# Optimization experiments

Measured on AMD Instinct MI355X. Metric: run time of the kernel, lower is better.

## Reference

```python
import jax, jax.numpy as jnp
import numpy as np

B, CHAR_LEN, LSTM, VOCAB, NATTN = 4096, 64, 400, 73, 10

def _lstm_cell(x, h, c, W_ih, W_hh, b):
    # gates: [B, 4*LSTM] in (i, f, g, o) order, matching torch.nn.LSTMCell
    g = x @ W_ih.T + h @ W_hh.T + b
    i, f, gg, o = jnp.split(g, 4, axis=1)
    i = jax.nn.sigmoid(i); f = jax.nn.sigmoid(f)
    gg = jnp.tanh(gg); o = jax.nn.sigmoid(o)
    c_new = f * c + i * gg
    h_new = o * jnp.tanh(c_new)
    return h_new, c_new

def setup_inputs() -> dict:
    key = jax.random.key(0)
    ks = jax.random.split(key, 24)
    d = {}
    d['inputs'] = jax.random.normal(ks[0], (B, 3), jnp.float32)
    for n, k in zip(['h1','c1','h2','c2','h3','c3'], ks[1:7]):
        d[n] = jax.random.normal(k, (B, LSTM), jnp.float32) * 0.1
    d['kappa'] = jax.random.uniform(ks[7], (B, NATTN), jnp.float32) * 5.0
    d['w_prev'] = jax.random.uniform(ks[8], (B, VOCAB), jnp.float32)
    d['attention_values'] = jax.random.uniform(ks[9], (B, CHAR_LEN, VOCAB), jnp.float32)
    d['attention_lengths'] = jax.random.randint(ks[10], (B,), 1, CHAR_LEN + 1, jnp.int32)
    s = 0.05
    in1 = VOCAB + 3              # lstm1 input: [w, inputs]
    in23 = 3 + LSTM + VOCAB      # lstm2/3 input: [inputs, h, w]
    attn_in = VOCAB + 3 + LSTM
    d['W_ih1'] = jax.random.normal(ks[11], (4 * LSTM, in1), jnp.float32) * s
    d['W_hh1'] = jax.random.normal(ks[12], (4 * LSTM, LSTM), jnp.float32) * s
    d['b1'] = jax.random.normal(ks[13], (4 * LSTM,), jnp.float32) * s
    d['W_attn'] = jax.random.normal(ks[14], (3 * NATTN, attn_in), jnp.float32) * s
    d['b_attn'] = jax.random.normal(ks[15], (3 * NATTN,), jnp.float32) * s
    d['W_ih2'] = jax.random.normal(ks[16], (4 * LSTM, in23), jnp.float32) * s
    d['W_hh2'] = jax.random.normal(ks[17], (4 * LSTM, LSTM), jnp.float32) * s
    d['b2'] = jax.random.normal(ks[18], (4 * LSTM,), jnp.float32) * s
    d['W_ih3'] = jax.random.normal(ks[19], (4 * LSTM, in23), jnp.float32) * s
    d['W_hh3'] = jax.random.normal(ks[20], (4 * LSTM, LSTM), jnp.float32) * s
    d['b3'] = jax.random.normal(ks[21], (4 * LSTM,), jnp.float32) * s
    return d

def reference(inputs, h1, c1, h2, c2, h3, c3, kappa, w_prev, attention_values,
              attention_lengths, W_ih1, W_hh1, b1, W_attn, b_attn,
              W_ih2, W_hh2, b2, W_ih3, W_hh3, b3):
    char_len = attention_values.shape[1]
    # --- LSTM 1 ---
    s1_in = jnp.concatenate([w_prev, inputs], axis=1)
    h1n, c1n = _lstm_cell(s1_in, h1, c1, W_ih1, W_hh1, b1)
    # --- Gaussian-mixture location attention ---
    attn_in = jnp.concatenate([w_prev, inputs, h1n], axis=1)
    attn_params = jax.nn.softplus(attn_in @ W_attn.T + b_attn)
    alpha, beta, kap = jnp.split(attn_params, 3, axis=1)
    kap = kappa + kap / 25.0
    beta = jnp.maximum(beta, 0.01)
    u = jnp.arange(char_len, dtype=jnp.float32)[None, None, :]           # [1,1,C]
    phi = jnp.sum(alpha[:, :, None] *
                  jnp.exp(-jnp.square(kap[:, :, None] - u) / beta[:, :, None]),
                  axis=1)                                                 # [B,C]
    seq_mask = (jnp.arange(char_len)[None, :] < attention_lengths[:, None]).astype(jnp.float32)
    w = jnp.einsum('bc,bcv->bv', phi * seq_mask, attention_values)        # [B,V]
    # --- LSTM 2 & 3 ---
    s2_in = jnp.concatenate([inputs, h1n, w], axis=1)
    h2n, c2n = _lstm_cell(s2_in, h2, c2, W_ih2, W_hh2, b2)
    s3_in = jnp.concatenate([inputs, h2n, w], axis=1)
    h3n, c3n = _lstm_cell(s3_in, h3, c3, W_ih3, W_hh3, b3)
    return h3n
```

## Files before the change

### kernel.cpp

```cpp
#include <hip/hip_runtime.h>
#include <hip/hip_bf16.h>


#define B_SZ     4096
#define LSTM_N   400
#define NG       1600
#define VOCAB    73
#define NATTN    10
#define CHARLEN  64
#define KP1      512
#define KP23     896

typedef _Float16 half8 __attribute__((ext_vector_type(8)));
typedef __attribute__((ext_vector_type(4))) float floatx4;

__device__ __forceinline__ void gload_lds16(const void* g, void* l) {
    __builtin_amdgcn_global_load_lds(
        (const __attribute__((address_space(1))) void*)g,
        (__attribute__((address_space(3))) void*)l, 16, 0, 0);
}

__device__ __forceinline__ int lds_off(int r, int g) {
    return (r << 6) + ((((g ^ r) & 7)) << 3);
}

__global__ __launch_bounds__(256) void pack_wall(const float* __restrict__ Wih1,
                                                 const float* __restrict__ Whh1,
                                                 const float* __restrict__ Wih2,
                                                 const float* __restrict__ Whh2,
                                                 const float* __restrict__ Wih3,
                                                 const float* __restrict__ Whh3,
                                                 const float* __restrict__ W_attn,
                                                 _Float16* __restrict__ W1,
                                                 _Float16* __restrict__ W2,
                                                 _Float16* __restrict__ W3,
                                                 _Float16* __restrict__ Wa)
{
    const int z = blockIdx.z;
    const int n = blockIdx.y;
    const int k = blockIdx.x * 256 + threadIdx.x;
    if (z == 3) {
        if (n >= 64 || k >= KP1) return;
        float v = (n < 30 && k < 476) ? W_attn[(size_t)n * 476 + k] : 0.f;
        Wa[(size_t)n * KP1 + k] = (_Float16)v;
        return;
    }
    if (n >= NG) return;
    const int u = n >> 2, g = n & 3;
    const int src = g * 400 + u;
    if (z == 0) {
        if (k >= KP1) return;
        float v = 0.f;
        if (k < 76)           v = Wih1[(size_t)src * 76 + k];
        else if (k < 476)     v = Whh1[(size_t)src * 400 + (k - 76)];
        W1[(size_t)n * KP1 + k] = (_Float16)v;
    } else {
        if (k >= KP23) return;
        const float* Wih = (z == 1) ? Wih2 : Wih3;
        const float* Whh = (z == 1) ? Whh2 : Whh3;
        float v = 0.f;
        if (k < 476)          v = Wih[(size_t)src * 476 + k];
        else if (k < 876)     v = Whh[(size_t)src * 400 + (k - 476)];
        ((z == 1) ? W2 : W3)[(size_t)n * KP23 + k] = (_Float16)v;
    }
}

__global__ __launch_bounds__(256) void pack_x(const float* __restrict__ w_prev,
                                              const float* __restrict__ inputs,
                                              const float* __restrict__ h1,
                                              const float* __restrict__ h2,
                                              const float* __restrict__ h3,
                                              _Float16* __restrict__ X1,
                                              _Float16* __restrict__ XA,
                                              _Float16* __restrict__ X2,
                                              _Float16* __restrict__ X3)
{
    const int b = blockIdx.y;
    const int k = blockIdx.x * 256 + threadIdx.x;
    if (k < KP1) {
        float v = 0.f;
        if (k < 73)        v = w_prev[(size_t)b * 73 + k];
        else if (k < 76)   v = inputs[(size_t)b * 3 + (k - 73)];
        else if (k < 476)  v = h1[(size_t)b * 400 + (k - 76)];
        X1[(size_t)b * KP1 + k] = (_Float16)v;
        if (k < 76 || k >= 476) XA[(size_t)b * KP1 + k] = (_Float16)v;
    }
    const int kk = k - KP1;
    if (kk >= 0 && kk < KP23) {
        if (kk >= 3 && kk < 476) return;
        float v2 = 0.f, v3 = 0.f;
        if (kk < 3) { v2 = inputs[(size_t)b * 3 + kk]; v3 = v2; }
        else if (kk >= 476 && kk < 876) {
            v2 = h2[(size_t)b * 400 + (kk - 476)];
            v3 = h3[(size_t)b * 400 + (kk - 476)];
        }
        X2[(size_t)b * KP23 + kk] = (_Float16)v2;
        X3[(size_t)b * KP23 + kk] = (_Float16)v3;
    }
}

__global__ __launch_bounds__(256) void gemm_fused(const _Float16* __restrict__ Wm,
                                                  const _Float16* __restrict__ X,
                                                  const float* __restrict__ bias,
                                                  const float* __restrict__ c_in,
                                                  _Float16* __restrict__ d1, int ld1,
                                                  _Float16* __restrict__ d2, int ld2,
                                                  float* __restrict__ fout, int Kp)
{
    __shared__ _Float16 As[64 * 64];
    __shared__ _Float16 Bs[128 * 64];

    const int t    = threadIdx.x;
    const int w    = t >> 6;
    const int lane = t & 63;
    const int quad = lane >> 4;
    const int l16  = lane & 15;
    const int m0   = blockIdx.y * 64;
    const int n0   = blockIdx.x * 128;
    const int wm   = (w >> 1) * 32;
    const int wn   = (w & 1) * 64;
    const int lr   = lane >> 3;
    const int gq   = (lane & 7) ^ lr;

    floatx4 acc[2][4] = {};

    for (int k0 = 0; k0 < Kp; k0 += 64) {
        __syncthreads();
        {
            const int cr = w * 16;
#pragma unroll
            for (int s = 0; s < 2; s++)
                gload_lds16(Wm + (size_t)(m0 + cr + s * 8 + lr) * Kp + k0 + gq * 8,
                            As + (cr + s * 8) * 64);
        }
#pragma unroll
        for (int j = 0; j < 2; j++) {
            const int cr = (j * 4 + w) * 16;
#pragma unroll
            for (int s = 0; s < 2; s++)
                gload_lds16(X + (size_t)(n0 + cr + s * 8 + lr) * Kp + k0 + gq * 8,
                            Bs + (cr + s * 8) * 64);
        }
        asm volatile("s_waitcnt vmcnt(0)" ::: "memory");
        __syncthreads();

#pragma unroll
        for (int h = 0; h < 2; h++) {
            half8 af[2], bf[4];
#pragma unroll
            for (int i = 0; i < 2; i++)
                af[i] = *(const half8*)(As + lds_off(wm + i * 16 + l16, h * 4 + quad));
#pragma unroll
            for (int i = 0; i < 4; i++)
                bf[i] = *(const half8*)(Bs + lds_off(wn + i * 16 + l16, h * 4 + quad));
#pragma unroll
            for (int mt = 0; mt < 2; mt++)
#pragma unroll
                for (int nt = 0; nt < 4; nt++)
                    acc[mt][nt] = __builtin_amdgcn_mfma_f32_16x16x32_f16(
                        af[mt], bf[nt], acc[mt][nt], 0, 0, 0);
        }
    }

#pragma unroll
    for (int mt = 0; mt < 2; mt++) {
        const int u = ((m0 + wm + mt * 16) >> 2) + quad;
        const float bi  = bias[u];
        const float bff = bias[400 + u];
        const float bg  = bias[800 + u];
        const float bo  = bias[1200 + u];
#pragma unroll
        for (int nt = 0; nt < 4; nt++) {
            const int b = n0 + wn + nt * 16 + l16;
            float gi = acc[mt][nt][0] + bi;
            float gf = acc[mt][nt][1] + bff;
            float gg = acc[mt][nt][2] + bg;
            float go = acc[mt][nt][3] + bo;
            float si = 1.f / (1.f + expf(-gi));
            float sf = 1.f / (1.f + expf(-gf));
            float so = 1.f / (1.f + expf(-go));
            float cn = sf * c_in[(size_t)b * LSTM_N + u] + si * tanhf(gg);
            float h  = so * tanhf(cn);
            if (fout) {
                fout[(size_t)b * LSTM_N + u] = h;
            } else {
                _Float16 hh = (_Float16)h;
                d1[(size_t)b * ld1 + u] = hh;
                if (d2) d2[(size_t)b * ld2 + u] = hh;
            }
        }
    }
}

__global__ __launch_bounds__(256) void gemm_plain(const _Float16* __restrict__ Wa,
                                                  const _Float16* __restrict__ XA,
                                                  const float* __restrict__ bias,
                                                  float* __restrict__ C, int Kp)
{
    __shared__ _Float16 As[64 * 64];
    __shared__ _Float16 Bs[128 * 64];

    const int t    = threadIdx.x;
    const int w    = t >> 6;
    const int lane = t & 63;
    const int quad = lane >> 4;
    const int l16  = lane & 15;
    const int n0   = blockIdx.x * 128;
    const int wm   = (w >> 1) * 32;
    const int wn   = (w & 1) * 64;
    const int lr   = lane >> 3;
    const int gq   = (lane & 7) ^ lr;

    floatx4 acc[2][4] = {};

    for (int k0 = 0; k0 < Kp; k0 += 64) {
        __syncthreads();
        {
            const int cr = w * 16;
#pragma unroll
            for (int s = 0; s < 2; s++)
                gload_lds16(Wa + (size_t)(cr + s * 8 + lr) * Kp + k0 + gq * 8,
                            As + (cr + s * 8) * 64);
        }
#pragma unroll
        for (int j = 0; j < 2; j++) {
            const int cr = (j * 4 + w) * 16;
#pragma unroll
            for (int s = 0; s < 2; s++)
                gload_lds16(XA + (size_t)(n0 + cr + s * 8 + lr) * Kp + k0 + gq * 8,
                            Bs + (cr + s * 8) * 64);
        }
        asm volatile("s_waitcnt vmcnt(0)" ::: "memory");
        __syncthreads();

#pragma unroll
        for (int h = 0; h < 2; h++) {
            half8 af[2], bf[4];
#pragma unroll
            for (int i = 0; i < 2; i++)
                af[i] = *(const half8*)(As + lds_off(wm + i * 16 + l16, h * 4 + quad));
#pragma unroll
            for (int i = 0; i < 4; i++)
                bf[i] = *(const half8*)(Bs + lds_off(wn + i * 16 + l16, h * 4 + quad));
#pragma unroll
            for (int mt = 0; mt < 2; mt++)
#pragma unroll
                for (int nt = 0; nt < 4; nt++)
                    acc[mt][nt] = __builtin_amdgcn_mfma_f32_16x16x32_f16(
                        af[mt], bf[nt], acc[mt][nt], 0, 0, 0);
        }
    }

#pragma unroll
    for (int mt = 0; mt < 2; mt++) {
#pragma unroll
        for (int r = 0; r < 4; r++) {
            const int m = wm + mt * 16 + quad * 4 + r;
            if (m >= 30) continue;
            const float bv = bias[m];
#pragma unroll
            for (int nt = 0; nt < 4; nt++) {
                const int b = n0 + wn + nt * 16 + l16;
                C[(size_t)b * 32 + m] = acc[mt][nt][r] + bv;
            }
        }
    }
}

__global__ __launch_bounds__(256) void attn_phi(const float* __restrict__ AP,
                                                const float* __restrict__ kappa,
                                                const float* __restrict__ AV,
                                                const int* __restrict__ alen,
                                                _Float16* __restrict__ X2,
                                                _Float16* __restrict__ X3)
{
    __shared__ float prm[4][32];
    __shared__ float phi_s[4][CHARLEN];

    const int t = threadIdx.x;
    const int wave = t >> 6;
    const int lane = t & 63;
    const int b = blockIdx.x * 4 + wave;

    if (lane < 30) {
        float p  = AP[(size_t)b * 32 + lane];
        float sp = (p > 20.f) ? p : log1pf(expf(p));
        float v;
        if (lane < 10)      v = sp;
        else if (lane < 20) v = fmaxf(sp, 0.01f);
        else                v = kappa[(size_t)b * NATTN + (lane - 20)] + sp * (1.f / 25.f);
        prm[wave][lane] = v;
    }
    __syncthreads();

    const int len = alen[b];
    {
        int c = lane;
        float phi = 0.f;
#pragma unroll
        for (int j = 0; j < NATTN; j++) {
            float d = prm[wave][20 + j] - (float)c;
            phi += prm[wave][j] * expf(-d * d / prm[wave][10 + j]);
        }
        phi_s[wave][c] = (c < len) ? phi : 0.f;
    }
    __syncthreads();

    for (int v0 = 0; v0 < VOCAB; v0 += 64) {
        const int v = v0 + lane;
        if (v < VOCAB) {
            const float* avb = AV + (size_t)b * CHARLEN * VOCAB + v;
            float s = 0.f;
            for (int c = 0; c < len; c++)
                s += phi_s[wave][c] * avb[(size_t)c * VOCAB];
            _Float16 wv = (_Float16)s;
            X2[(size_t)b * KP23 + 403 + v] = wv;
            X3[(size_t)b * KP23 + 403 + v] = wv;
        }
    }
}

extern "C" void kernel_launch(void* const* d_in, const int* in_sizes, int n_in,
                              void* d_out, int out_size, void* d_ws, size_t ws_size,
                              hipStream_t stream)
{
    const float* inputs = (const float*)d_in[0];
    const float* h1     = (const float*)d_in[1];
    const float* c1     = (const float*)d_in[2];
    const float* h2     = (const float*)d_in[3];
    const float* c2     = (const float*)d_in[4];
    const float* h3     = (const float*)d_in[5];
    const float* c3     = (const float*)d_in[6];
    const float* kappa  = (const float*)d_in[7];
    const float* w_prev = (const float*)d_in[8];
    const float* AV     = (const float*)d_in[9];
    const int*   alen   = (const int*)d_in[10];
    const float* W_ih1  = (const float*)d_in[11];
    const float* W_hh1  = (const float*)d_in[12];
    const float* b1     = (const float*)d_in[13];
    const float* W_attn = (const float*)d_in[14];
    const float* b_attn = (const float*)d_in[15];
    const float* W_ih2  = (const float*)d_in[16];
    const float* W_hh2  = (const float*)d_in[17];
    const float* b2     = (const float*)d_in[18];
    const float* W_ih3  = (const float*)d_in[19];
    const float* W_hh3  = (const float*)d_in[20];
    const float* b3     = (const float*)d_in[21];
    float* out = (float*)d_out;

    char* p = (char*)d_ws;
    _Float16* X1 = (_Float16*)p; p += (size_t)B_SZ * KP1 * 2;
    _Float16* XA = (_Float16*)p; p += (size_t)B_SZ * KP1 * 2;
    _Float16* X2 = (_Float16*)p; p += (size_t)B_SZ * KP23 * 2;
    _Float16* X3 = (_Float16*)p; p += (size_t)B_SZ * KP23 * 2;
    _Float16* W1 = (_Float16*)p; p += (size_t)NG * KP1 * 2;
    _Float16* W2 = (_Float16*)p; p += (size_t)NG * KP23 * 2;
    _Float16* W3 = (_Float16*)p; p += (size_t)NG * KP23 * 2;
    _Float16* Wa = (_Float16*)p; p += (size_t)64 * KP1 * 2;
    float* AP = (float*)p;

    pack_wall<<<dim3(4, NG, 4), 256, 0, stream>>>(W_ih1, W_hh1, W_ih2, W_hh2,
                                                  W_ih3, W_hh3, W_attn,
                                                  W1, W2, W3, Wa);
    pack_x<<<dim3((KP1 + KP23 + 255) / 256, B_SZ), 256, 0, stream>>>(
        w_prev, inputs, h1, h2, h3, X1, XA, X2, X3);

    const dim3 fgrid(B_SZ / 128, NG / 64);

    gemm_fused<<<fgrid, 256, 0, stream>>>(W1, X1, b1, c1,
                                          XA + 76, KP1, X2 + 3, KP23, nullptr, KP1);
    gemm_plain<<<dim3(B_SZ / 128, 1), 256, 0, stream>>>(Wa, XA, b_attn, AP, KP1);
    attn_phi<<<B_SZ / 4, 256, 0, stream>>>(AP, kappa, AV, alen, X2, X3);
    gemm_fused<<<fgrid, 256, 0, stream>>>(W2, X2, b2, c2,
                                          X3 + 3, KP23, nullptr, 0, nullptr, KP23);
    gemm_fused<<<fgrid, 256, 0, stream>>>(W3, X3, b3, c3,
                                          nullptr, 0, nullptr, 0, out, KP23);
}
```

Before: 298.7 us.

## Double-buffer LDS tiles in GEMM kernels and template on K

Converts the fused LSTM GEMM and the attention GEMM to a two-stage LDS ping-pong. The next K tile is loaded directly to LDS while MFMAs run on the current one, with a partial vmcnt wait. K becomes a compile-time template parameter so the K loop fully unrolls. This doubles LDS use per block (to 48KB), which may lower occupancy and raise register pressure from the unrolling.

```diff
diff --git a/kernel.cpp b/kernel.cpp
--- a/kernel.cpp
+++ b/kernel.cpp
@@ -99,16 +99,17 @@
     }
 }
 
-__global__ __launch_bounds__(256) void gemm_fused(const _Float16* __restrict__ Wm,
-                                                  const _Float16* __restrict__ X,
-                                                  const float* __restrict__ bias,
-                                                  const float* __restrict__ c_in,
-                                                  _Float16* __restrict__ d1, int ld1,
-                                                  _Float16* __restrict__ d2, int ld2,
-                                                  float* __restrict__ fout, int Kp)
-{
-    __shared__ _Float16 As[64 * 64];
-    __shared__ _Float16 Bs[128 * 64];
+template<int KP>
+__global__ __launch_bounds__(256) void gemm_fused_t(const _Float16* __restrict__ Wm,
+                                                    const _Float16* __restrict__ X,
+                                                    const float* __restrict__ bias,
+                                                    const float* __restrict__ c_in,
+                                                    _Float16* __restrict__ d1, int ld1,
+                                                    _Float16* __restrict__ d2, int ld2,
+                                                    float* __restrict__ fout)
+{
+    __shared__ _Float16 As[2][64 * 64];
+    __shared__ _Float16 Bs[2][128 * 64];
 
     const int t    = threadIdx.x;
     const int w    = t >> 6;
@@ -124,35 +125,45 @@
 
     floatx4 acc[2][4] = {};
 
-    for (int k0 = 0; k0 < Kp; k0 += 64) {
-        __syncthreads();
-        {
-            const int cr = w * 16;
+    auto stage = [&](int sb, int k0) {
+        const int cr = w * 16;
+#pragma unroll
+        for (int s = 0; s < 2; s++)
+            gload_lds16(Wm + (size_t)(m0 + cr + s * 8 + lr) * KP + k0 + gq * 8,
+                        &As[sb][(cr + s * 8) * 64]);
+#pragma unroll
+        for (int j = 0; j < 2; j++) {
+            const int cr2 = (j * 4 + w) * 16;
 #pragma unroll
             for (int s = 0; s < 2; s++)
-                gload_lds16(Wm + (size_t)(m0 + cr + s * 8 + lr) * Kp + k0 + gq * 8,
-                            As + (cr + s * 8) * 64);
-        }
-#pragma unroll
-        for (int j = 0; j < 2; j++) {
-            const int cr = (j * 4 + w) * 16;
-#pragma unroll
-            for (int s = 0; s < 2; s++)
-                gload_lds16(X + (size_t)(n0 + cr + s * 8 + lr) * Kp + k0 + gq * 8,
-                            Bs + (cr + s * 8) * 64);
-        }
-        asm volatile("s_waitcnt vmcnt(0)" ::: "memory");
-        __syncthreads();
+                gload_lds16(X + (size_t)(n0 + cr2 + s * 8 + lr) * KP + k0 + gq * 8,
+                            &Bs[sb][(cr2 + s * 8) * 64]);
+        }
+    };
+
+    stage(0, 0);
+    constexpr int NT = KP / 64;
+#pragma unroll
+    for (int kt = 0; kt < NT; kt++) {
+        const int sb = kt & 1;
+        if (kt + 1 < NT) {
+            stage(sb ^ 1, (kt + 1) * 64);
+            asm volatile("s_waitcnt vmcnt(6)" ::: "memory");
+        } else {
+            asm volatile("s_waitcnt vmcnt(0)" ::: "memory");
+        }
+        __builtin_amdgcn_s_barrier();
+        __builtin_amdgcn_sched_barrier(0);
 
 #pragma unroll
         for (int h = 0; h < 2; h++) {
             half8 af[2], bf[4];
 #pragma unroll
             for (int i = 0; i < 2; i++)
-                af[i] = *(const half8*)(As + lds_off(wm + i * 16 + l16, h * 4 + quad));
+                af[i] = *(const half8*)(&As[sb][lds_off(wm + i * 16 + l16, h * 4 + quad)]);
 #pragma unroll
             for (int i = 0; i < 4; i++)
-                bf[i] = *(const half8*)(Bs + lds_off(wn + i * 16 + l16, h * 4 + quad));
+                bf[i] = *(const half8*)(&Bs[sb][lds_off(wn + i * 16 + l16, h * 4 + quad)]);
 #pragma unroll
             for (int mt = 0; mt < 2; mt++)
 #pragma unroll
@@ -160,6 +171,7 @@
                     acc[mt][nt] = __builtin_amdgcn_mfma_f32_16x16x32_f16(
                         af[mt], bf[nt], acc[mt][nt], 0, 0, 0);
         }
+        __builtin_amdgcn_s_barrier();
     }
 
 #pragma unroll
@@ -195,10 +207,10 @@
 __global__ __launch_bounds__(256) void gemm_plain(const _Float16* __restrict__ Wa,
                                                   const _Float16* __restrict__ XA,
                                                   const float* __restrict__ bias,
-                                                  float* __restrict__ C, int Kp)
-{
-    __shared__ _Float16 As[64 * 64];
-    __shared__ _Float16 Bs[128 * 64];
+                                                  float* __restrict__ C)
+{
+    __shared__ _Float16 As[2][64 * 64];
+    __shared__ _Float16 Bs[2][128 * 64];
 
     const int t    = threadIdx.x;
     const int w    = t >> 6;
@@ -213,35 +225,45 @@
 
     floatx4 acc[2][4] = {};
 
-    for (int k0 = 0; k0 < Kp; k0 += 64) {
-        __syncthreads();
-        {
-            const int cr = w * 16;
+    auto stage = [&](int sb, int k0) {
+        const int cr = w * 16;
+#pragma unroll
+        for (int s = 0; s < 2; s++)
+            gload_lds16(Wa + (size_t)(cr + s * 8 + lr) * KP1 + k0 + gq * 8,
+                        &As[sb][(cr + s * 8) * 64]);
+#pragma unroll
+        for (int j = 0; j < 2; j++) {
+            const int cr2 = (j * 4 + w) * 16;
 #pragma unroll
             for (int s = 0; s < 2; s++)
-                gload_lds16(Wa + (size_t)(cr + s * 8 + lr) * Kp + k0 + gq * 8,
-                            As + (cr + s * 8) * 64);
-        }
-#pragma unroll
-        for (int j = 0; j < 2; j++) {
-            const int cr = (j * 4 + w) * 16;
-#pragma unroll
-            for (int s = 0; s < 2; s++)
-                gload_lds16(XA + (size_t)(n0 + cr + s * 8 + lr) * Kp + k0 + gq * 8,
-                            Bs + (cr + s * 8) * 64);
-        }
-        asm volatile("s_waitcnt vmcnt(0)" ::: "memory");
-        __syncthreads();
+                gload_lds16(XA + (size_t)(n0 + cr2 + s * 8 + lr) * KP1 + k0 + gq * 8,
+                            &Bs[sb][(cr2 + s * 8) * 64]);
+        }
+    };
+
+    stage(0, 0);
+    constexpr int NT = KP1 / 64;
+#pragma unroll
+    for (int kt = 0; kt < NT; kt++) {
+        const int sb = kt & 1;
+        if (kt + 1 < NT) {
+            stage(sb ^ 1, (kt + 1) * 64);
+            asm volatile("s_waitcnt vmcnt(6)" ::: "memory");
+        } else {
+            asm volatile("s_waitcnt vmcnt(0)" ::: "memory");
+        }
+        __builtin_amdgcn_s_barrier();
+        __builtin_amdgcn_sched_barrier(0);
 
 #pragma unroll
         for (int h = 0; h < 2; h++) {
             half8 af[2], bf[4];
 #pragma unroll
             for (int i = 0; i < 2; i++)
-                af[i] = *(const half8*)(As + lds_off(wm + i * 16 + l16, h * 4 + quad));
+                af[i] = *(const half8*)(&As[sb][lds_off(wm + i * 16 + l16, h * 4 + quad)]);
 #pragma unroll
             for (int i = 0; i < 4; i++)
-                bf[i] = *(const half8*)(Bs + lds_off(wn + i * 16 + l16, h * 4 + quad));
+                bf[i] = *(const half8*)(&Bs[sb][lds_off(wn + i * 16 + l16, h * 4 + quad)]);
 #pragma unroll
             for (int mt = 0; mt < 2; mt++)
 #pragma unroll
@@ -249,6 +271,7 @@
                     acc[mt][nt] = __builtin_amdgcn_mfma_f32_16x16x32_f16(
                         af[mt], bf[nt], acc[mt][nt], 0, 0, 0);
         }
+        __builtin_amdgcn_s_barrier();
     }
 
 #pragma unroll
@@ -367,12 +390,12 @@
 
     const dim3 fgrid(B_SZ / 128, NG / 64);
 
-    gemm_fused<<<fgrid, 256, 0, stream>>>(W1, X1, b1, c1,
-                                          XA + 76, KP1, X2 + 3, KP23, nullptr, KP1);
-    gemm_plain<<<dim3(B_SZ / 128, 1), 256, 0, stream>>>(Wa, XA, b_attn, AP, KP1);
+    gemm_fused_t<KP1><<<fgrid, 256, 0, stream>>>(W1, X1, b1, c1,
+                                                 XA + 76, KP1, X2 + 3, KP23, nullptr);
+    gemm_plain<<<dim3(B_SZ / 128, 1), 256, 0, stream>>>(Wa, XA, b_attn, AP);
     attn_phi<<<B_SZ / 4, 256, 0, stream>>>(AP, kappa, AV, alen, X2, X3);
-    gemm_fused<<<fgrid, 256, 0, stream>>>(W2, X2, b2, c2,
-                                          X3 + 3, KP23, nullptr, 0, nullptr, KP23);
-    gemm_fused<<<fgrid, 256, 0, stream>>>(W3, X3, b3, c3,
-                                          nullptr, 0, nullptr, 0, out, KP23);
-}
+    gemm_fused_t<KP23><<<fgrid, 256, 0, stream>>>(W2, X2, b2, c2,
+                                                  X3 + 3, KP23, nullptr, 0, nullptr);
+    gemm_fused_t<KP23><<<fgrid, 256, 0, stream>>>(W3, X3, b3, c3,
+                                                  nullptr, 0, nullptr, 0, out);
+}
```

After: 309.8 us. +3.7%, slower.
